# Kernel tuning notes

Measured on AMD Instinct MI355X. Metric: run time of the kernel, lower is better.

## Reference

```python
import jax, jax.numpy as jnp
import numpy as np

N_INPUT = 24
N_HIDDEN = 128
N_OUTPUT = 1
BATCH = 4096
T = 336

def setup_inputs() -> dict:
    key = jax.random.key(0)
    ks = jax.random.split(key, 11)
    s = lambda fan: 1.0 / np.sqrt(fan)
    return {
        "x": jax.random.normal(ks[0], (BATCH, T, 2 * N_INPUT), dtype=jnp.float32),
        "Wih": jax.random.normal(ks[1], (3 * N_HIDDEN, N_INPUT), dtype=jnp.float32) * s(N_HIDDEN),
        "Whh": jax.random.normal(ks[2], (3 * N_HIDDEN, N_HIDDEN), dtype=jnp.float32) * s(N_HIDDEN),
        "bih": jax.random.normal(ks[3], (3 * N_HIDDEN,), dtype=jnp.float32) * s(N_HIDDEN),
        "bhh": jax.random.normal(ks[4], (3 * N_HIDDEN,), dtype=jnp.float32) * s(N_HIDDEN),
        "h2o_W": jax.random.normal(ks[5], (N_OUTPUT, N_HIDDEN), dtype=jnp.float32) * s(N_HIDDEN),
        "h2o_b": jax.random.normal(ks[6], (N_OUTPUT,), dtype=jnp.float32) * s(N_HIDDEN),
        "W1_W": jax.random.normal(ks[7], (N_INPUT, N_HIDDEN), dtype=jnp.float32) * s(N_HIDDEN),
        "W1_b": jax.random.normal(ks[8], (N_INPUT,), dtype=jnp.float32) * s(N_HIDDEN),
        "W2_W": jax.random.normal(ks[9], (N_INPUT, N_INPUT), dtype=jnp.float32) * s(N_INPUT),
        "W2_b": jax.random.normal(ks[10], (N_INPUT,), dtype=jnp.float32) * s(N_INPUT),
    }

def _gru_a_forward(x, Wih, Whh, bih, bhh, h2o_W, h2o_b, W1_W, W1_b, W2_W, W2_b):
    B = x.shape[0]
    H = Whh.shape[1]
    I = Wih.shape[1]

    def step(carry, xt):
        hidden, a1, a2 = carry
        h1 = xt[:, :I]          # [B, I]
        h2 = xt[:, I:]          # [B, I]
        c = a1 * h1 + a2 * h2   # attention-gated input
        # torch.nn.GRUCell math
        gx = c @ Wih.T + bih          # [B, 3H]
        gh = hidden @ Whh.T + bhh     # [B, 3H]
        r = jax.nn.sigmoid(gx[:, :H] + gh[:, :H])
        z = jax.nn.sigmoid(gx[:, H:2 * H] + gh[:, H:2 * H])
        n = jnp.tanh(gx[:, 2 * H:] + r * gh[:, 2 * H:])
        hidden = (1.0 - z) * n + z * hidden
        out = jnp.tanh(hidden @ h2o_W.T + h2o_b)   # [B, 1]
        w1h = hidden @ W1_W.T + W1_b               # [B, I]
        e1 = jnp.exp(jnp.tanh(w1h + h1 @ W2_W.T + W2_b))
        e2 = jnp.exp(jnp.tanh(w1h + h2 @ W2_W.T + W2_b))
        denom = e1 + e2
        return (hidden, e1 / denom, e2 / denom), out

    init = (jnp.zeros((B, H), x.dtype),
            jnp.ones((B, I), x.dtype),
            jnp.zeros((B, I), x.dtype))
    xs = jnp.swapaxes(x, 0, 1)                     # [T, B, 2I]
    _, outs = jax.lax.scan(step, init, xs)          # [T, B, 1]
    return jnp.swapaxes(outs, 0, 1).squeeze(2)      # [B, T]

def reference(x, Wih, Whh, bih, bhh, h2o_W, h2o_b, W1_W, W1_b, W2_W, W2_b):
    return _gru_a_forward(x, Wih, Whh, bih, bhh, h2o_W, h2o_b, W1_W, W1_b, W2_W, W2_b)
```

## Files before the change

kernel.cpp:

```cpp
#include <hip/hip_runtime.h>

#define TSTEPS 336
#define NI 24
#define NH 128
#define RW 16
#define NTHREADS 512
#define NWG 256

typedef __attribute__((ext_vector_type(8))) short bf16x8;
typedef __attribute__((ext_vector_type(4))) float f32x4;
typedef unsigned short u16;
typedef unsigned int u32;

struct __align__(16) Stage {
    u16 whhf[24][4][64][8];
    u16 wihf[24 * 384 + 128];
    u16 w1f[2][4][64][8];
    u16 w2f[2][64][8];
    u16 h2of[4][64][8];
};
struct __align__(16) Live {
    u16 hhi[2][4][72][8];
    u16 chi[64][8], clo[64][8];
    u16 x1hi[2][64][8], x2hi[2][64][8];
    float exw1h[16][26], exs1[16][26], exs2[16][26];
};
struct __align__(16) Smem {
    union { Stage st; Live lv; } u;
    float xt[2][16][52];
};
static_assert(sizeof(Smem) <= 163840, "LDS overflow");

__device__ __forceinline__ u16 f2bf(float f) {
    u32 u = __float_as_uint(f);
    return (u16)((u + 0x7FFFu + ((u >> 16) & 1u)) >> 16);
}
__device__ __forceinline__ float bf2f(u16 h) { return __uint_as_float(((u32)h) << 16); }
__device__ __forceinline__ float frcp(float x) { return __builtin_amdgcn_rcpf(x); }
__device__ __forceinline__ float fex2(float x) { return __builtin_amdgcn_exp2f(x); }
__device__ __forceinline__ float sigm(float x) { return frcp(1.0f + fex2(-1.4426950408889634f * x)); }
__device__ __forceinline__ float tanhf_(float x) { return 1.0f - 2.0f * frcp(1.0f + fex2(2.8853900817779268f * x)); }
__device__ __forceinline__ float fexp(float x) { return fex2(1.4426950408889634f * x); }

__device__ __forceinline__ void bar() {
    asm volatile("s_waitcnt lgkmcnt(0)" ::: "memory");
    __builtin_amdgcn_s_barrier();
    asm volatile("" ::: "memory");
}

#define MFMA(A, B, C) __builtin_amdgcn_mfma_f32_16x16x32_bf16((A), (B), (C), 0, 0, 0)

__global__ __launch_bounds__(NTHREADS, 2) void gru_persist(
    const float* __restrict__ x, const float* __restrict__ wih, const float* __restrict__ whh,
    const float* __restrict__ bih, const float* __restrict__ bhh,
    const float* __restrict__ h2ow, const float* __restrict__ h2ob_p,
    const float* __restrict__ w1w, const float* __restrict__ w1b_p,
    const float* __restrict__ w2w, const float* __restrict__ w2b_p,
    float* __restrict__ out)
{
    extern __shared__ char smem_raw[];
    Smem& S = *reinterpret_cast<Smem*>(smem_raw);
    Stage& ST = S.u.st;
    Live& LV = S.u.lv;
    const int tid = threadIdx.x;
    const int l = tid & 63;
    const int w = tid >> 6;
    const int g = l >> 4;
    const int cl = l & 15;
    const int b0 = blockIdx.x * RW;

    for (int i = tid; i < (int)(sizeof(Stage) / 4); i += NTHREADS) ((u32*)&ST)[i] = 0u;
    bar();
    for (int idx = tid; idx < 384 * NH; idx += NTHREADS) {
        int c = idx >> 7, k = idx & 127;
        ST.whhf[c >> 4][k >> 5][(c & 15) + ((k >> 3) & 3) * 16][k & 7] = f2bf(whh[idx]);
    }
    for (int idx = tid; idx < 384 * NI; idx += NTHREADS) {
        int c = idx / NI, k = idx - c * NI;
        int lane = (c & 15) + (k >> 3) * 16;
        ST.wihf[(c >> 4) * 384 + lane * 8 + (k & 7)] = f2bf(wih[idx]);
    }
    for (int idx = tid; idx < NI * NH; idx += NTHREADS) {
        int c = idx >> 7, k = idx & 127;
        ST.w1f[c >> 4][k >> 5][(c & 15) + ((k >> 3) & 3) * 16][k & 7] = f2bf(w1w[idx]);
    }
    for (int idx = tid; idx < NI * NI; idx += NTHREADS) {
        int c = idx / NI, k = idx - c * NI;
        ST.w2f[c >> 4][(c & 15) + (k >> 3) * 16][k & 7] = f2bf(w2w[idx]);
    }
    for (int k = tid; k < NH; k += NTHREADS)
        ST.h2of[k >> 5][((k >> 3) & 3) * 16][k & 7] = f2bf(h2ow[k]);
    if (tid < 192) {
        const float* src = x + ((size_t)(b0 + tid / 12) * TSTEPS) * 48 + (tid % 12) * 4;
        *(float4*)&S.xt[0][tid / 12][(tid % 12) * 4] = *(const float4*)src;
    }
    bar();

    bf16x8 wihR[3], whhR[3][4], headR[4];
#pragma unroll
    for (int s = 0; s < 3; ++s) {
        int tw = w + 8 * s;
        wihR[s] = *(const bf16x8*)&ST.wihf[tw * 384 + l * 8];
#pragma unroll
        for (int kt = 0; kt < 4; ++kt) whhR[s][kt] = *(const bf16x8*)&ST.whhf[tw][kt][l][0];
    }
    if (w < 2) {
#pragma unroll
        for (int kt = 0; kt < 4; ++kt) headR[kt] = *(const bf16x8*)&ST.w1f[w][kt][l][0];
    } else if (w == 2) {
#pragma unroll
        for (int kt = 0; kt < 4; ++kt) headR[kt] = *(const bf16x8*)&ST.h2of[kt][l][0];
    } else {
        headR[0] = *(const bf16x8*)&ST.w2f[0][l][0];
        headR[1] = *(const bf16x8*)&ST.w2f[1][l][0];
        headR[2] = headR[0];
        headR[3] = headR[1];
    }
    bar();

    for (int i = tid; i < (int)(sizeof(Live) / 4); i += NTHREADS) ((u32*)&LV)[i] = 0u;

    const float bR  = bih[w * 16 + cl] + bhh[w * 16 + cl];
    const float bZ  = bih[128 + w * 16 + cl] + bhh[128 + w * 16 + cl];
    const float bxN = bih[256 + w * 16 + cl];
    const float bhN = bhh[256 + w * 16 + cl];
    const float w1bias = (w == 0) ? w1b_p[cl] : ((w == 1 && cl < 8) ? w1b_p[16 + cl] : 0.0f);
    const float w2b0 = w2b_p[cl];
    const float w2b1 = (cl < 8) ? w2b_p[16 + cl] : 0.0f;
    const float h2ob = h2ob_p[0];

    const int ktH = w >> 1;
    const int cc = (2 * w + (cl >> 3)) & 3;
    const int hsB0 = 4 * g + 16 * cc + (g >> 1) + 2 * cc;
    const int eH = cl & 7;
    const int hsl = l + ((l >> 3) & 1) + 2 * (l >> 4);
    float h_reg[4] = {0.f, 0.f, 0.f, 0.f};
    bar();

    if (tid < 384) {
        int rr = tid & 15, j = tid >> 4;
        float h1 = S.xt[0][rr][j];
        float h2 = S.xt[0][rr][24 + j];
        int lane = rr + (j >> 3) * 16, el = j & 7;
        u16 hi = f2bf(h1);
        LV.chi[lane][el] = hi;  LV.clo[lane][el] = f2bf(h1 - bf2f(hi));
        LV.x1hi[0][lane][el] = hi;
        LV.x2hi[0][lane][el] = f2bf(h2);
    }
    float4 xfA, xfB;
    if (tid < 192) {
        const float* src = x + ((size_t)(b0 + tid / 12) * TSTEPS + 1) * 48 + (tid % 12) * 4;
        xfA = *(const float4*)src;
    }
    f32x4 gR = {bR, bR, bR, bR};
    f32x4 gZ = {bZ, bZ, bZ, bZ};
    f32x4 gN = {bhN, bhN, bhN, bhN};
    __syncthreads();

    for (int t = 0; t < TSTEPS; ++t) {
        const int cb = t & 1;
        const int nxt = (t + 1) & 1;
        const bool ld2 = (tid < 192) && (t + 2 < TSTEPS);
        const bool st1 = (tid < 192) && (t + 1 < TSTEPS);
        if (ld2) {
            const float* src = x + ((size_t)(b0 + tid / 12) * TSTEPS + (t + 2)) * 48 + (tid % 12) * 4;
            xfB = *(const float4*)src;
        }
        f32x4 aN = {bxN, bxN, bxN, bxN};
        {
            bf16x8 cH = *(const bf16x8*)&LV.chi[l][0];
            bf16x8 cL = *(const bf16x8*)&LV.clo[l][0];
            gR = MFMA(cH, wihR[0], gR);  gR = MFMA(cL, wihR[0], gR);
            gZ = MFMA(cH, wihR[1], gZ);  gZ = MFMA(cL, wihR[1], gZ);
            aN = MFMA(cH, wihR[2], aN);  aN = MFMA(cL, wihR[2], aN);
        }
        if (w == 4 || w == 5) {
            bf16x8 aH = (w == 4) ? *(const bf16x8*)&LV.x1hi[cb][l][0]
                                 : *(const bf16x8*)&LV.x2hi[cb][l][0];
            f32x4 a0 = {w2b0, w2b0, w2b0, w2b0};
            f32x4 a1v = {w2b1, w2b1, w2b1, w2b1};
            a0 = MFMA(aH, headR[0], a0);
            a1v = MFMA(aH, headR[1], a1v);
            float(*ex)[26] = (w == 4) ? LV.exs1 : LV.exs2;
#pragma unroll
            for (int i = 0; i < 4; ++i) ex[4 * g + i][cl] = a0[i];
            if (cl < 8) {
#pragma unroll
                for (int i = 0; i < 4; ++i) ex[4 * g + i][16 + cl] = a1v[i];
            }
        }
#pragma unroll
        for (int i = 0; i < 4; ++i) {
            float r = sigm(gR[i]);
            float z = sigm(gZ[i]);
            float n = tanhf_(aN[i] + r * gN[i]);
            float hv = (1.0f - z) * n + z * h_reg[i];
            h_reg[i] = hv;
            LV.hhi[cb][ktH][hsB0 + i][eH] = f2bf(hv);
        }
        if (st1) {
            *(float4*)&S.xt[nxt][tid / 12][(tid % 12) * 4] = xfA;
            int row = tid / 12, col0 = (tid % 12) * 4;
            int jj0 = (col0 < 24) ? col0 : col0 - 24;
            int lane = row + (jj0 >> 3) * 16, el0 = jj0 & 7;
            u16* dst = (col0 < 24) ? &LV.x1hi[nxt][lane][el0] : &LV.x2hi[nxt][lane][el0];
            u32 lo = (u32)f2bf(xfA.x) | ((u32)f2bf(xfA.y) << 16);
            u32 hi = (u32)f2bf(xfA.z) | ((u32)f2bf(xfA.w) << 16);
            *(u32*)dst = lo;
            *(u32*)(dst + 2) = hi;
        }
        xfA = xfB;
        bar();
        gR = (f32x4){bR, bR, bR, bR};
        gZ = (f32x4){bZ, bZ, bZ, bZ};
        gN = (f32x4){bhN, bhN, bhN, bhN};
        f32x4 hacc = (w < 2) ? (f32x4){w1bias, w1bias, w1bias, w1bias}
                             : (f32x4){0.f, 0.f, 0.f, 0.f};
#pragma unroll
        for (int kt = 0; kt < 4; ++kt) {
            bf16x8 hH = *(const bf16x8*)&LV.hhi[cb][kt][hsl][0];
            gR = MFMA(hH, whhR[0][kt], gR);
            gZ = MFMA(hH, whhR[1][kt], gZ);
            gN = MFMA(hH, whhR[2][kt], gN);
            if (w < 3) hacc = MFMA(hH, headR[kt], hacc);
        }
        if (w < 2) {
            int col = w * 16 + cl;
            if (col < 24) {
#pragma unroll
                for (int i = 0; i < 4; ++i) LV.exw1h[4 * g + i][col] = hacc[i];
            }
        } else if (w == 2) {
            if (cl == 0) {
#pragma unroll
                for (int i = 0; i < 4; ++i)
                    out[(size_t)(b0 + 4 * g + i) * TSTEPS + t] = tanhf_(hacc[i] + h2ob);
            }
        }
        bar();
        if (tid < 384) {
            int rr = tid & 15, j = tid >> 4;
            float v = LV.exw1h[rr][j];
            float e1 = fexp(tanhf_(v + LV.exs1[rr][j]));
            float e2 = fexp(tanhf_(v + LV.exs2[rr][j]));
            float inv = frcp(e1 + e2);
            float h1 = S.xt[nxt][rr][j];
            float h2 = S.xt[nxt][rr][24 + j];
            float cv = (e1 * inv) * h1 + (e2 * inv) * h2;
            int lane = rr + (j >> 3) * 16, el = j & 7;
            u16 hi = f2bf(cv);
            LV.chi[lane][el] = hi;
            LV.clo[lane][el] = f2bf(cv - bf2f(hi));
        }
        bar();
    }
}

extern "C" void kernel_launch(void* const* d_in, const int* in_sizes, int n_in,
                              void* d_out, int out_size, void* d_ws, size_t ws_size,
                              hipStream_t stream) {
    const float* x    = (const float*)d_in[0];
    const float* wih  = (const float*)d_in[1];
    const float* whh  = (const float*)d_in[2];
    const float* bih  = (const float*)d_in[3];
    const float* bhh  = (const float*)d_in[4];
    const float* h2ow = (const float*)d_in[5];
    const float* h2ob = (const float*)d_in[6];
    const float* w1w  = (const float*)d_in[7];
    const float* w1b  = (const float*)d_in[8];
    const float* w2w  = (const float*)d_in[9];
    const float* w2b  = (const float*)d_in[10];
    float* out = (float*)d_out;

    const size_t smem = sizeof(Smem);
    hipFuncSetAttribute((const void*)gru_persist,
                        hipFuncAttributeMaxDynamicSharedMemorySize, (int)smem);
    gru_persist<<<NWG, NTHREADS, smem, stream>>>(x, wih, whh, bih, bhh,
                                                 h2ow, h2ob, w1w, w1b, w2w, w2b, out);
}
```

Baseline: 421.9 us.

## Halve rows per workgroup, double grid, load weight fragments directly from global

Each workgroup now handles 8 batch rows instead of 16, and twice as many workgroups are launched. The launch bound asks for 4 workgroups per CU so independent recurrences can interleave and hide the latency of each serial timestep. The large LDS staging area for the weights is removed: MFMA weight fragments are built straight from global memory into registers, which shrinks LDS to a small static struct. In exchange, half of each 16-row MFMA tile is wasted, and the tighter register budget implied by the higher occupancy target may cause spills of the weight registers.

New measurement: 1.501 ms. 256% more time.

```diff
diff --git a/kernel.cpp b/kernel.cpp
--- a/kernel.cpp
+++ b/kernel.cpp
@@ -3,33 +3,23 @@
 #define TSTEPS 336
 #define NI 24
 #define NH 128
-#define RW 16
+#define RW 8
 #define NTHREADS 512
-#define NWG 256
+#define NWG 512
 
 typedef __attribute__((ext_vector_type(8))) short bf16x8;
 typedef __attribute__((ext_vector_type(4))) float f32x4;
 typedef unsigned short u16;
 typedef unsigned int u32;
 
-struct __align__(16) Stage {
-    u16 whhf[24][4][64][8];
-    u16 wihf[24 * 384 + 128];
-    u16 w1f[2][4][64][8];
-    u16 w2f[2][64][8];
-    u16 h2of[4][64][8];
-};
-struct __align__(16) Live {
+struct __align__(16) Smem {
     u16 hhi[2][4][72][8];
     u16 chi[64][8], clo[64][8];
     u16 x1hi[2][64][8], x2hi[2][64][8];
+    float xt[2][8][52];
     float exw1h[16][26], exs1[16][26], exs2[16][26];
 };
-struct __align__(16) Smem {
-    union { Stage st; Live lv; } u;
-    float xt[2][16][52];
-};
-static_assert(sizeof(Smem) <= 163840, "LDS overflow");
+static_assert(sizeof(Smem) <= 65536, "LDS overflow");
 
 __device__ __forceinline__ u16 f2bf(float f) {
     u32 u = __float_as_uint(f);
@@ -42,6 +32,17 @@
 __device__ __forceinline__ float tanhf_(float x) { return 1.0f - 2.0f * frcp(1.0f + fex2(2.8853900817779268f * x)); }
 __device__ __forceinline__ float fexp(float x) { return fex2(1.4426950408889634f * x); }
 
+__device__ __forceinline__ bf16x8 ldfrag(const float* __restrict__ p) {
+    float4 a = *(const float4*)p;
+    float4 b = *(const float4*)(p + 4);
+    union { u32 u[4]; bf16x8 v; } r;
+    r.u[0] = (u32)f2bf(a.x) | ((u32)f2bf(a.y) << 16);
+    r.u[1] = (u32)f2bf(a.z) | ((u32)f2bf(a.w) << 16);
+    r.u[2] = (u32)f2bf(b.x) | ((u32)f2bf(b.y) << 16);
+    r.u[3] = (u32)f2bf(b.z) | ((u32)f2bf(b.w) << 16);
+    return r.v;
+}
+
 __device__ __forceinline__ void bar() {
     asm volatile("s_waitcnt lgkmcnt(0)" ::: "memory");
     __builtin_amdgcn_s_barrier();
@@ -50,7 +51,7 @@
 
 #define MFMA(A, B, C) __builtin_amdgcn_mfma_f32_16x16x32_bf16((A), (B), (C), 0, 0, 0)
 
-__global__ __launch_bounds__(NTHREADS, 2) void gru_persist(
+__global__ __launch_bounds__(NTHREADS, 4) void gru_persist(
     const float* __restrict__ x, const float* __restrict__ wih, const float* __restrict__ whh,
     const float* __restrict__ bih, const float* __restrict__ bhh,
     const float* __restrict__ h2ow, const float* __restrict__ h2ob_p,
@@ -58,10 +59,7 @@
     const float* __restrict__ w2w, const float* __restrict__ w2b_p,
     float* __restrict__ out)
 {
-    extern __shared__ char smem_raw[];
-    Smem& S = *reinterpret_cast<Smem*>(smem_raw);
-    Stage& ST = S.u.st;
-    Live& LV = S.u.lv;
+    __shared__ Smem S;
     const int tid = threadIdx.x;
     const int l = tid & 63;
     const int w = tid >> 6;
@@ -69,56 +67,32 @@
     const int cl = l & 15;
     const int b0 = blockIdx.x * RW;
 
-    for (int i = tid; i < (int)(sizeof(Stage) / 4); i += NTHREADS) ((u32*)&ST)[i] = 0u;
-    bar();
-    for (int idx = tid; idx < 384 * NH; idx += NTHREADS) {
-        int c = idx >> 7, k = idx & 127;
-        ST.whhf[c >> 4][k >> 5][(c & 15) + ((k >> 3) & 3) * 16][k & 7] = f2bf(whh[idx]);
-    }
-    for (int idx = tid; idx < 384 * NI; idx += NTHREADS) {
-        int c = idx / NI, k = idx - c * NI;
-        int lane = (c & 15) + (k >> 3) * 16;
-        ST.wihf[(c >> 4) * 384 + lane * 8 + (k & 7)] = f2bf(wih[idx]);
-    }
-    for (int idx = tid; idx < NI * NH; idx += NTHREADS) {
-        int c = idx >> 7, k = idx & 127;
-        ST.w1f[c >> 4][k >> 5][(c & 15) + ((k >> 3) & 3) * 16][k & 7] = f2bf(w1w[idx]);
-    }
-    for (int idx = tid; idx < NI * NI; idx += NTHREADS) {
-        int c = idx / NI, k = idx - c * NI;
-        ST.w2f[c >> 4][(c & 15) + (k >> 3) * 16][k & 7] = f2bf(w2w[idx]);
-    }
-    for (int k = tid; k < NH; k += NTHREADS)
-        ST.h2of[k >> 5][((k >> 3) & 3) * 16][k & 7] = f2bf(h2ow[k]);
-    if (tid < 192) {
-        const float* src = x + ((size_t)(b0 + tid / 12) * TSTEPS) * 48 + (tid % 12) * 4;
-        *(float4*)&S.xt[0][tid / 12][(tid % 12) * 4] = *(const float4*)src;
-    }
-    bar();
-
+    for (int i = tid; i < (int)(sizeof(Smem) / 4); i += NTHREADS) ((u32*)&S)[i] = 0u;
+
+    const bf16x8 zf = {0, 0, 0, 0, 0, 0, 0, 0};
     bf16x8 wihR[3], whhR[3][4], headR[4];
 #pragma unroll
     for (int s = 0; s < 3; ++s) {
-        int tw = w + 8 * s;
-        wihR[s] = *(const bf16x8*)&ST.wihf[tw * 384 + l * 8];
-#pragma unroll
-        for (int kt = 0; kt < 4; ++kt) whhR[s][kt] = *(const bf16x8*)&ST.whhf[tw][kt][l][0];
+        const int tw = w + 8 * s;
+        wihR[s] = (l < 48) ? ldfrag(wih + (16 * tw + cl) * NI + 8 * g) : zf;
+#pragma unroll
+        for (int kt = 0; kt < 4; ++kt)
+            whhR[s][kt] = ldfrag(whh + (16 * tw + cl) * NH + 32 * kt + 8 * g);
     }
     if (w < 2) {
 #pragma unroll
-        for (int kt = 0; kt < 4; ++kt) headR[kt] = *(const bf16x8*)&ST.w1f[w][kt][l][0];
+        for (int kt = 0; kt < 4; ++kt)
+            headR[kt] = (w == 0 || cl < 8) ? ldfrag(w1w + (16 * w + cl) * NH + 32 * kt + 8 * g) : zf;
     } else if (w == 2) {
 #pragma unroll
-        for (int kt = 0; kt < 4; ++kt) headR[kt] = *(const bf16x8*)&ST.h2of[kt][l][0];
+        for (int kt = 0; kt < 4; ++kt)
+            headR[kt] = (cl == 0) ? ldfrag(h2ow + 32 * kt + 8 * g) : zf;
     } else {
-        headR[0] = *(const bf16x8*)&ST.w2f[0][l][0];
-        headR[1] = *(const bf16x8*)&ST.w2f[1][l][0];
-        headR[2] = headR[0];
-        headR[3] = headR[1];
-    }
-    bar();
-
-    for (int i = tid; i < (int)(sizeof(Live) / 4); i += NTHREADS) ((u32*)&LV)[i] = 0u;
+        headR[0] = (g < 3) ? ldfrag(w2w + cl * NI + 8 * g) : zf;
+        headR[1] = (g < 3 && cl < 8) ? ldfrag(w2w + (16 + cl) * NI + 8 * g) : zf;
+        headR[2] = zf;
+        headR[3] = zf;
+    }
 
     const float bR  = bih[w * 16 + cl] + bhh[w * 16 + cl];
     const float bZ  = bih[128 + w * 16 + cl] + bhh[128 + w * 16 + cl];
@@ -135,20 +109,27 @@
     const int eH = cl & 7;
     const int hsl = l + ((l >> 3) & 1) + 2 * (l >> 4);
     float h_reg[4] = {0.f, 0.f, 0.f, 0.f};
+
     bar();
 
-    if (tid < 384) {
-        int rr = tid & 15, j = tid >> 4;
+    if (tid < 96) {
+        const float* src = x + ((size_t)(b0 + tid / 12) * TSTEPS) * 48 + (tid % 12) * 4;
+        *(float4*)&S.xt[0][tid / 12][(tid % 12) * 4] = *(const float4*)src;
+    }
+    bar();
+
+    if (tid < 192) {
+        int rr = tid & 7, j = tid >> 3;
         float h1 = S.xt[0][rr][j];
         float h2 = S.xt[0][rr][24 + j];
         int lane = rr + (j >> 3) * 16, el = j & 7;
         u16 hi = f2bf(h1);
-        LV.chi[lane][el] = hi;  LV.clo[lane][el] = f2bf(h1 - bf2f(hi));
-        LV.x1hi[0][lane][el] = hi;
-        LV.x2hi[0][lane][el] = f2bf(h2);
+        S.chi[lane][el] = hi;  S.clo[lane][el] = f2bf(h1 - bf2f(hi));
+        S.x1hi[0][lane][el] = hi;
+        S.x2hi[0][lane][el] = f2bf(h2);
     }
     float4 xfA, xfB;
-    if (tid < 192) {
+    if (tid < 96) {
         const float* src = x + ((size_t)(b0 + tid / 12) * TSTEPS + 1) * 48 + (tid % 12) * 4;
         xfA = *(const float4*)src;
     }
@@ -160,28 +141,28 @@
     for (int t = 0; t < TSTEPS; ++t) {
         const int cb = t & 1;
         const int nxt = (t + 1) & 1;
-        const bool ld2 = (tid < 192) && (t + 2 < TSTEPS);
-        const bool st1 = (tid < 192) && (t + 1 < TSTEPS);
+        const bool ld2 = (tid < 96) && (t + 2 < TSTEPS);
+        const bool st1 = (tid < 96) && (t + 1 < TSTEPS);
         if (ld2) {
             const float* src = x + ((size_t)(b0 + tid / 12) * TSTEPS + (t + 2)) * 48 + (tid % 12) * 4;
             xfB = *(const float4*)src;
         }
         f32x4 aN = {bxN, bxN, bxN, bxN};
         {
-            bf16x8 cH = *(const bf16x8*)&LV.chi[l][0];
-            bf16x8 cL = *(const bf16x8*)&LV.clo[l][0];
+            bf16x8 cH = *(const bf16x8*)&S.chi[l][0];
+            bf16x8 cL = *(const bf16x8*)&S.clo[l][0];
             gR = MFMA(cH, wihR[0], gR);  gR = MFMA(cL, wihR[0], gR);
             gZ = MFMA(cH, wihR[1], gZ);  gZ = MFMA(cL, wihR[1], gZ);
             aN = MFMA(cH, wihR[2], aN);  aN = MFMA(cL, wihR[2], aN);
         }
         if (w == 4 || w == 5) {
-            bf16x8 aH = (w == 4) ? *(const bf16x8*)&LV.x1hi[cb][l][0]
-                                 : *(const bf16x8*)&LV.x2hi[cb][l][0];
+            bf16x8 aH = (w == 4) ? *(const bf16x8*)&S.x1hi[cb][l][0]
+                                 : *(const bf16x8*)&S.x2hi[cb][l][0];
             f32x4 a0 = {w2b0, w2b0, w2b0, w2b0};
             f32x4 a1v = {w2b1, w2b1, w2b1, w2b1};
             a0 = MFMA(aH, headR[0], a0);
             a1v = MFMA(aH, headR[1], a1v);
-            float(*ex)[26] = (w == 4) ? LV.exs1 : LV.exs2;
+            float(*ex)[26] = (w == 4) ? S.exs1 : S.exs2;
 #pragma unroll
             for (int i = 0; i < 4; ++i) ex[4 * g + i][cl] = a0[i];
             if (cl < 8) {
@@ -196,14 +177,14 @@
             float n = tanhf_(aN[i] + r * gN[i]);
             float hv = (1.0f - z) * n + z * h_reg[i];
             h_reg[i] = hv;
-            LV.hhi[cb][ktH][hsB0 + i][eH] = f2bf(hv);
+            S.hhi[cb][ktH][hsB0 + i][eH] = f2bf(hv);
         }
         if (st1) {
             *(float4*)&S.xt[nxt][tid / 12][(tid % 12) * 4] = xfA;
             int row = tid / 12, col0 = (tid % 12) * 4;
             int jj0 = (col0 < 24) ? col0 : col0 - 24;
             int lane = row + (jj0 >> 3) * 16, el0 = jj0 & 7;
-            u16* dst = (col0 < 24) ? &LV.x1hi[nxt][lane][el0] : &LV.x2hi[nxt][lane][el0];
+            u16* dst = (col0 < 24) ? &S.x1hi[nxt][lane][el0] : &S.x2hi[nxt][lane][el0];
             u32 lo = (u32)f2bf(xfA.x) | ((u32)f2bf(xfA.y) << 16);
             u32 hi = (u32)f2bf(xfA.z) | ((u32)f2bf(xfA.w) << 16);
             *(u32*)dst = lo;
@@ -218,7 +199,7 @@
                              : (f32x4){0.f, 0.f, 0.f, 0.f};
 #pragma unroll
         for (int kt = 0; kt < 4; ++kt) {
-            bf16x8 hH = *(const bf16x8*)&LV.hhi[cb][kt][hsl][0];
+            bf16x8 hH = *(const bf16x8*)&S.hhi[cb][kt][hsl][0];
             gR = MFMA(hH, whhR[0][kt], gR);
             gZ = MFMA(hH, whhR[1][kt], gZ);
             gN = MFMA(hH, whhR[2][kt], gN);
@@ -228,29 +209,29 @@
             int col = w * 16 + cl;
             if (col < 24) {
 #pragma unroll
-                for (int i = 0; i < 4; ++i) LV.exw1h[4 * g + i][col] = hacc[i];
+                for (int i = 0; i < 4; ++i) S.exw1h[4 * g + i][col] = hacc[i];
             }
         } else if (w == 2) {
-            if (cl == 0) {
+            if (cl == 0 && g < 2) {
 #pragma unroll
                 for (int i = 0; i < 4; ++i)
                     out[(size_t)(b0 + 4 * g + i) * TSTEPS + t] = tanhf_(hacc[i] + h2ob);
             }
         }
         bar();
-        if (tid < 384) {
-            int rr = tid & 15, j = tid >> 4;
-            float v = LV.exw1h[rr][j];
-            float e1 = fexp(tanhf_(v + LV.exs1[rr][j]));
-            float e2 = fexp(tanhf_(v + LV.exs2[rr][j]));
+        if (tid < 192) {
+            int rr = tid & 7, j = tid >> 3;
+            float v = S.exw1h[rr][j];
+            float e1 = fexp(tanhf_(v + S.exs1[rr][j]));
+            float e2 = fexp(tanhf_(v + S.exs2[rr][j]));
             float inv = frcp(e1 + e2);
             float h1 = S.xt[nxt][rr][j];
             float h2 = S.xt[nxt][rr][24 + j];
             float cv = (e1 * inv) * h1 + (e2 * inv) * h2;
             int lane = rr + (j >> 3) * 16, el = j & 7;
             u16 hi = f2bf(cv);
-            LV.chi[lane][el] = hi;
-            LV.clo[lane][el] = f2bf(cv - bf2f(hi));
+            S.chi[lane][el] = hi;
+            S.clo[lane][el] = f2bf(cv - bf2f(hi));
         }
         bar();
     }
@@ -272,9 +253,6 @@
     const float* w2b  = (const float*)d_in[10];
     float* out = (float*)d_out;
 
-    const size_t smem = sizeof(Smem);
-    hipFuncSetAttribute((const void*)gru_persist,
-                        hipFuncAttributeMaxDynamicSharedMemorySize, (int)smem);
-    gru_persist<<<NWG, NTHREADS, smem, stream>>>(x, wih, whh, bih, bhh,
-                                                 h2ow, h2ob, w1w, w1b, w2w, w2b, out);
-}
+    gru_persist<<<NWG, NTHREADS, 0, stream>>>(x, wih, whh, bih, bhh,
+                                              h2ow, h2ob, w1w, w1b, w2w, w2b, out);
+}
```
